# Optimization experiments

Hardware: AMD Instinct MI355X
Metric: run time of the kernel (lower is better)

The kernel has to match this reference:

```python
import jax, jax.numpy as jnp
import numpy as np
from jax import lax

B, H, W, C = 8, 72, 72, 16
HID_E, HID_P, T = 128, 16, 64
P_EPS = 1e-06
ALIVE_TH = 0.1

# Sobel kernels. The torch code runs conv on NCHW with spatial dims (D2, D1)
# (x.transpose(1,3)); in our NHWC layout spatial dims are (D1, D2), so the
# equivalent kernel is the transpose. With angle=0: w1 = dx, w2 = dy = dx.T.
_DX = np.outer([1.0, 2.0, 1.0], [-1.0, 0.0, 1.0]) / 8.0
_W1_EFF = _DX.T            # transpose of w1
_W2_EFF = _DX              # transpose of w2 (= dy.T)


def _depthwise(x, k2d):
    c = x.shape[-1]
    ker = jnp.tile(jnp.asarray(k2d, x.dtype)[:, :, None, None], (1, 1, 1, c))  # HWIO (3,3,1,C)
    return lax.conv_general_dilated(x, ker, (1, 1), 'SAME',
                                    feature_group_count=c,
                                    dimension_numbers=('NHWC', 'HWIO', 'NHWC'))


def _conv2d(x, w, b):
    y = lax.conv_general_dilated(x, w, (1, 1), 'SAME',
                                 dimension_numbers=('NHWC', 'HWIO', 'NHWC'))
    return y + b


def _maxpool3(a):  # a: (B,H,W)
    return lax.reduce_window(a, -jnp.inf, lax.max, (1, 3, 3), (1, 1, 1),
                             [(0, 0), (1, 1), (1, 1)])


def setup_inputs() -> dict:
    key = jax.random.key(0)
    ks = jax.random.split(key, 6)
    c3 = 3 * C
    x = jax.random.uniform(ks[0], (B, H, W, C), jnp.float32)
    conv1_w = jax.random.normal(ks[1], (3, 3, c3, HID_P), jnp.float32) * (1.0 / np.sqrt(9 * c3))
    conv1_b = jnp.zeros((HID_P,), jnp.float32)
    conv2_w = jax.random.normal(ks[2], (3, 3, HID_P, 1), jnp.float32) * (1.0 / np.sqrt(9 * HID_P))
    conv2_b = jnp.zeros((1,), jnp.float32)
    fc0_w = jax.random.normal(ks[3], (c3, HID_E), jnp.float32) * (1.0 / np.sqrt(c3))
    fc0_b = jnp.zeros((HID_E,), jnp.float32)
    fc1_w = jax.random.normal(ks[4], (HID_E, C), jnp.float32) * 0.01  # torch init is zeros; small random for a non-degenerate baseline
    return dict(x=x, conv1_w=conv1_w, conv1_b=conv1_b, conv2_w=conv2_w,
                conv2_b=conv2_b, fc0_w=fc0_w, fc0_b=fc0_b, fc1_w=fc1_w)


def reference(x, conv1_w, conv1_b, conv2_w, conv2_b, fc0_w, fc0_b, fc1_w):
    base_key = jax.random.key(42)

    def perceive(x):  # (B,H,W,C) -> (B,H,W,3C)
        return jnp.concatenate([x, _depthwise(x, _W1_EFF), _depthwise(x, _W2_EFF)], axis=-1)

    def lambda_net(perc):  # (B,H,W,3C) -> (B,H,W)
        h = jax.nn.relu(_conv2d(perc, conv1_w, conv1_b))
        return jax.nn.sigmoid(_conv2d(h, conv2_w, conv2_b))[..., 0]

    def alive(x):  # alpha channel index 3
        return _maxpool3(x[..., 3]) > ALIVE_TH

    def update(x, lambdas, key):
        pre = alive(x)
        perc = perceive(x)
        dx = jax.nn.relu(perc @ fc0_w + fc0_b) @ fc1_w  # pointwise MLP, fc1 has no bias
        upd = 1.0 - jax.random.bernoulli(key, lambdas).astype(x.dtype)  # (B,H,W)
        xn = x + dx * upd[..., None]
        life = (pre & alive(xn)).astype(x.dtype)[..., None]
        return xn * life, upd, perc

    # initial perceive/lambda/update (step 0)
    perc0 = perceive(x)
    lam0 = lambda_net(perc0)
    x0, upd0, perc = update(x, lam0, jax.random.fold_in(base_key, 0))
    un0 = jnp.ones((x.shape[0], H, W), x.dtype)

    def step(carry, n):
        xc, updc, percc, un = carry
        lam = lambda_net(percc)
        p_n = un * lam + P_EPS
        out = (xc, p_n, lam, updc)
        un = un * (1.0 - lam)
        xn, updn, percn = update(xc, lam, jax.random.fold_in(base_key, n))
        return (xn, updn, percn, un), out

    _, (x_steps, p_steps, lam_steps, upd_steps) = lax.scan(
        step, (x0, upd0, perc, un0), jnp.arange(1, T + 1))
    p_norm = p_steps / jnp.sum(p_steps, axis=0)
    return x_steps, p_norm, lam_steps, upd_steps
```

## Files before the change

kernel.cpp:

```cpp
#include <hip/hip_runtime.h>
#include <cstdint>
#include <cmath>

#define B_    8
#define H_    72
#define W_    72
#define C_    16
#define C3_   48
#define HP_   16
#define HE_   128
#define T_    64
#define NCELL 41472
#define NEDGE 2272

__host__ __device__ __forceinline__ void threefry2x32(uint32_t k0, uint32_t k1,
                                                      uint32_t& x0, uint32_t& x1) {
  uint32_t ks2 = k0 ^ k1 ^ 0x1BD11BDAu;
  x0 += k0; x1 += k1;
#define TF_R(r) { x0 += x1; x1 = (x1 << (r)) | (x1 >> (32 - (r))); x1 ^= x0; }
  TF_R(13) TF_R(15) TF_R(26) TF_R(6)
  x0 += k1; x1 += ks2 + 1u;
  TF_R(17) TF_R(29) TF_R(16) TF_R(24)
  x0 += ks2; x1 += k0 + 2u;
  TF_R(13) TF_R(15) TF_R(26) TF_R(6)
  x0 += k0; x1 += k1 + 3u;
  TF_R(17) TF_R(29) TF_R(16) TF_R(24)
  x0 += k1; x1 += ks2 + 4u;
  TF_R(13) TF_R(15) TF_R(26) TF_R(6)
  x0 += ks2; x1 += k0 + 5u;
#undef TF_R
}

__global__ void k_init(const float* __restrict__ xin, double* __restrict__ xA,
                       double* __restrict__ un) {
  int idx = blockIdx.x * 256 + threadIdx.x;
  if (idx < NCELL * C_) xA[idx] = (double)xin[idx];
  if (idx < NCELL) un[idx] = 1.0;
}

__global__ void k_prep(const float* __restrict__ w1, const float* __restrict__ b1,
                       const float* __restrict__ f0w, const float* __restrict__ f0b,
                       const float* __restrict__ f1w, const float* __restrict__ w2,
                       double* __restrict__ weffd, double* __restrict__ b1d,
                       double* __restrict__ fc0t, double* __restrict__ fc1d,
                       double* __restrict__ w2d, double* __restrict__ f0bd,
                       double* __restrict__ w1d) {
  int gid = blockIdx.x * 256 + threadIdx.x;
  const int stride = 26 * 256;
  for (int t = gid; t < 6400; t += stride) {
    int oc = t & 15;
    int c  = (t >> 4) & 15;
    int pos = t >> 8;
    int u = pos / 5, v = pos % 5;
    double acc = 0.0;
    for (int ei = 0; ei < 3; ei++) {
      int di = u - ei; if (di < 0 || di > 2) continue;
      for (int ej = 0; ej < 3; ej++) {
        int dj = v - ej; if (dj < 0 || dj > 2) continue;
        const float* wb = w1 + (size_t)((ei * 3 + ej) * C3_) * HP_ + oc;
        if (di == 1 && dj == 1) acc += (double)wb[c * HP_];
        double rf1 = (di == 0) ? -0.125 : (di == 2) ? 0.125 : 0.0;
        if (rf1 != 0.0) {
          double cf1 = (dj == 1) ? 2.0 : 1.0;
          acc += (double)wb[(C_ + c) * HP_] * (rf1 * cf1);
        }
        double cf2 = (dj == 0) ? -0.125 : (dj == 2) ? 0.125 : 0.0;
        if (cf2 != 0.0) {
          double rf2 = (di == 1) ? 2.0 : 1.0;
          acc += (double)wb[(2 * C_ + c) * HP_] * (cf2 * rf2);
        }
      }
    }
    weffd[t] = acc;
  }
  for (int t = gid; t < C3_ * HE_; t += stride) {
    int k = t >> 7, e = t & 127;
    fc0t[e * C3_ + k] = (double)f0w[t];
  }
  for (int t = gid; t < HE_ * C_; t += stride) fc1d[t] = (double)f1w[t];
  for (int t = gid; t < 144; t += stride) w2d[t] = (double)w2[t];
  for (int t = gid; t < HE_; t += stride) f0bd[t] = (double)f0b[t];
  for (int t = gid; t < HP_; t += stride) b1d[t] = (double)b1[t];
  for (int t = gid; t < 3 * 3 * C3_ * HP_; t += stride) w1d[t] = (double)w1[t];
}

__global__ void __launch_bounds__(256) k_conv1(const double* __restrict__ x,
    const double* __restrict__ weffd, const double* __restrict__ b1d,
    const double* __restrict__ w1d, double* __restrict__ hbuf) {
  int lane = threadIdx.x & 63;
  int wv = __builtin_amdgcn_readfirstlane(threadIdx.x >> 6);
  if (blockIdx.x < 324) {
    int gw = blockIdx.x * 4 + wv;
    int cellw = gw >> 1;
    int ocb = (gw & 1) << 3;
    int cell = (cellw << 6) + lane;
    int j = cell % W_; int t2 = cell / W_; int i = t2 % H_; int b = t2 / H_;
    if (i == 0 || i == H_ - 1 || j == 0 || j == W_ - 1) return;
    double acc[8];
#pragma unroll
    for (int o = 0; o < 8; o++) acc[o] = b1d[ocb + o];
#pragma unroll 1
    for (int u = 0; u < 5; u++) {
      int ii = i + u - 2; if (ii < 0 || ii >= H_) continue;
#pragma unroll 1
      for (int v = 0; v < 5; v++) {
        int jj = j + v - 2; if (jj < 0 || jj >= W_) continue;
        const double* xp = x + ((size_t)((b * H_ + ii) * W_ + jj) << 4);
        const double* wp = weffd + (u * 5 + v) * 256 + ocb;
        double xv[16];
#pragma unroll
        for (int ic = 0; ic < 16; ic++) xv[ic] = xp[ic];
#pragma unroll
        for (int ic = 0; ic < 16; ic++) {
#pragma unroll
          for (int o = 0; o < 8; o++)
            acc[o] = fma(xv[ic], wp[ic * 16 + o], acc[o]);
        }
      }
    }
    double* hp = hbuf + ((size_t)cell << 4) + ocb;
#pragma unroll
    for (int o = 0; o < 8; o++) hp[o] = acc[o] > 0.0 ? acc[o] : 0.0;
  } else {
    int gw = (blockIdx.x - 324) * 4 + wv;
    int oc = gw & 15;
    int grp = gw >> 4;
    int ecell = (grp << 6) + lane;
    if (ecell >= NEDGE) return;
    int b = ecell / 284, r = ecell % 284;
    int i, j;
    if (r < 72)       { i = 0;       j = r; }
    else if (r < 144) { i = H_ - 1;  j = r - 72; }
    else if (r < 214) { i = r - 143; j = 0; }
    else              { i = r - 213; j = W_ - 1; }
    int cell = (b * H_ + i) * W_ + j;
    double acc = b1d[oc];
    for (int ei = 0; ei < 3; ei++) {
      int pi = i + ei - 1; if (pi < 0 || pi >= H_) continue;
      for (int ej = 0; ej < 3; ej++) {
        int pj = j + ej - 1; if (pj < 0 || pj >= W_) continue;
        const double* wb = w1d + (size_t)((ei * 3 + ej) * C3_) * HP_ + oc;
        for (int c = 0; c < C_; c++) {
          double v[3][3];
#pragma unroll
          for (int a2 = 0; a2 < 3; a2++) {
#pragma unroll
            for (int b2i = 0; b2i < 3; b2i++) {
              int ii2 = pi + a2 - 1, jj2 = pj + b2i - 1;
              bool ok = (ii2 >= 0 && ii2 < H_ && jj2 >= 0 && jj2 < W_);
              v[a2][b2i] = ok ? x[(((size_t)((b * H_ + ii2) * W_ + jj2)) << 4) + c] : 0.0;
            }
          }
          double ctr = v[1][1];
          double dw1 = (-v[0][0] - 2.0 * v[0][1] - v[0][2] + v[2][0] + 2.0 * v[2][1] + v[2][2]) * 0.125;
          double dw2 = (-v[0][0] + v[0][2] - 2.0 * v[1][0] + 2.0 * v[1][2] - v[2][0] + v[2][2]) * 0.125;
          acc += ctr * wb[c * HP_] + dw1 * wb[(C_ + c) * HP_] + dw2 * wb[(2 * C_ + c) * HP_];
        }
      }
    }
    hbuf[((size_t)cell << 4) + oc] = acc > 0.0 ? acc : 0.0;
  }
}

__global__ void __launch_bounds__(128) k_upd(
    const double* __restrict__ x, const double* __restrict__ hbuf,
    const double* __restrict__ lamPrev, const double* __restrict__ fc0t,
    const double* __restrict__ fc1d, const double* __restrict__ w2d,
    const double* __restrict__ f0bd, const float* __restrict__ b2,
    double* __restrict__ lamNext, double* __restrict__ xn,
    float* __restrict__ out_upd, double* __restrict__ un,
    float* __restrict__ out_lam, double* __restrict__ p_buf,
    uint32_t k0, uint32_t k1, int n) {
  __shared__ double sdx[64][17];
  int lane = threadIdx.x & 63;
  int wv = __builtin_amdgcn_readfirstlane(threadIdx.x >> 6);
  int cell = (blockIdx.x << 6) + lane;
  int j = cell % W_; int t2 = cell / W_; int i = t2 % H_; int b = t2 / H_;

  double pv[C3_];
#pragma unroll
  for (int k = 0; k < C3_; k++) pv[k] = 0.0;
#pragma unroll
  for (int p = 0; p < 9; p++) {
    const int di = p / 3, dj = p % 3;
    const double k1c = (di == 0 ? -0.125 : di == 2 ? 0.125 : 0.0) * (dj == 1 ? 2.0 : 1.0);
    const double k2c = (dj == 0 ? -0.125 : dj == 2 ? 0.125 : 0.0) * (di == 1 ? 2.0 : 1.0);
    int ii = i + di - 1, jj = j + dj - 1;
    if (ii < 0 || ii >= H_ || jj < 0 || jj >= W_) continue;
    const double* xp = x + ((size_t)((b * H_ + ii) * W_ + jj) << 4);
#pragma unroll
    for (int c = 0; c < C_; c++) {
      double xv = xp[c];
      if (p == 4) pv[c] += xv;
      if (k1c != 0.0) pv[C_ + c] = fma(k1c, xv, pv[C_ + c]);
      if (k2c != 0.0) pv[2 * C_ + c] = fma(k2c, xv, pv[2 * C_ + c]);
    }
  }

  double dx[C_];
#pragma unroll
  for (int c = 0; c < C_; c++) dx[c] = 0.0;
  int ebase = wv << 6;
#pragma unroll 2
  for (int eg = 0; eg < 64; eg += 4) {
    const double* wrow = fc0t + (size_t)(ebase + eg) * C3_;
    double a0 = f0bd[ebase + eg + 0];
    double a1 = f0bd[ebase + eg + 1];
    double a2 = f0bd[ebase + eg + 2];
    double a3 = f0bd[ebase + eg + 3];
#pragma unroll
    for (int k = 0; k < C3_; k++) {
      a0 = fma(pv[k], wrow[k], a0);
      a1 = fma(pv[k], wrow[C3_ + k], a1);
      a2 = fma(pv[k], wrow[2 * C3_ + k], a2);
      a3 = fma(pv[k], wrow[3 * C3_ + k], a3);
    }
    a0 = a0 > 0.0 ? a0 : 0.0;
    a1 = a1 > 0.0 ? a1 : 0.0;
    a2 = a2 > 0.0 ? a2 : 0.0;
    a3 = a3 > 0.0 ? a3 : 0.0;
    const double* v0 = fc1d + ((size_t)(ebase + eg) << 4);
#pragma unroll
    for (int c = 0; c < C_; c++) {
      double s = fma(a0, v0[c], dx[c]);
      s = fma(a1, v0[16 + c], s);
      s = fma(a2, v0[32 + c], s);
      s = fma(a3, v0[48 + c], s);
      dx[c] = s;
    }
  }

  if (wv == 1) {
#pragma unroll
    for (int c = 0; c < C_; c++) sdx[lane][c] = dx[c];
  }
  __syncthreads();
  if (wv == 1) return;

#pragma unroll
  for (int c = 0; c < C_; c++) dx[c] += sdx[lane][c];

  double z = (double)b2[0];
  for (int di = 0; di < 3; di++) {
    int ii = i + di - 1; if (ii < 0 || ii >= H_) continue;
    for (int dj = 0; dj < 3; dj++) {
      int jj = j + dj - 1; if (jj < 0 || jj >= W_) continue;
      const double* hh = hbuf + ((size_t)((b * H_ + ii) * W_ + jj) << 4);
      const double* ww = w2d + (di * 3 + dj) * HP_;
#pragma unroll
      for (int ic = 0; ic < HP_; ic++) z = fma(hh[ic], ww[ic], z);
    }
  }
  double lamF = 1.0 / (1.0 + exp(-z));
  lamNext[cell] = lamF;
  double l = (n == 0) ? lamF : lamPrev[cell];

  if (n >= 1) {
    size_t o = (size_t)(n - 1) * NCELL + cell;
    out_lam[o] = (float)l;
    double u = un[cell];
    p_buf[o] = u * l + 1e-6;
    un[cell] = u * (1.0 - l);
  }

  uint32_t r0 = 0u, r1 = (uint32_t)cell;
  threefry2x32(k0, k1, r0, r1);
  double uf = (double)(r0 ^ r1) * 0x1p-32;
  double upd = (uf < l) ? 0.0 : 1.0;
  out_upd[(size_t)n * NCELL + cell] = (float)upd;
  const double* xc = x + ((size_t)cell << 4);
  double* xo = xn + ((size_t)cell << 4);
#pragma unroll
  for (int c = 0; c < C_; c++) xo[c] = xc[c] + dx[c] * upd;
}

__global__ void k_life(const double* __restrict__ xold, const double* __restrict__ xn,
                       double* __restrict__ xout, float* __restrict__ out_x, int n) {
  int idx = blockIdx.x * 256 + threadIdx.x;
  int c = idx & 15;
  int cell = idx >> 4;
  int j = cell % W_; int t = cell / W_; int i = t % H_; int b = t / H_;
  double mo = -1e300, mn2 = -1e300;
  for (int di = -1; di <= 1; di++) {
    int ii = i + di; if (ii < 0 || ii >= H_) continue;
    for (int dj = -1; dj <= 1; dj++) {
      int jj = j + dj; if (jj < 0 || jj >= W_) continue;
      size_t nb = (size_t)((b * H_ + ii) * W_ + jj) * C_;
      double a0 = xold[nb + 3]; if (a0 > mo) mo = a0;
      double a1 = xn[nb + 3];   if (a1 > mn2) mn2 = a1;
    }
  }
  bool life = (mo > 0.1) && (mn2 > 0.1);
  double v = life ? xn[((size_t)cell << 4) + c] : 0.0;
  xout[((size_t)cell << 4) + c] = v;
  out_x[(size_t)n * NCELL * C_ + ((size_t)cell << 4) + c] = (float)v;
}

__global__ void k_emit(const double* __restrict__ lam, const double* __restrict__ un,
                       float* __restrict__ out_lam, double* __restrict__ p_buf) {
  int cell = blockIdx.x * 256 + threadIdx.x;
  double l = lam[cell];
  size_t o = (size_t)(T_ - 1) * NCELL + cell;
  out_lam[o] = (float)l;
  p_buf[o] = un[cell] * l + 1e-6;
}

__global__ void k_pnorm(const double* __restrict__ p_buf, float* __restrict__ out_p) {
  int cell = blockIdx.x * 256 + threadIdx.x;
  double s = 0.0;
  for (int t = 0; t < T_; t++) s += p_buf[(size_t)t * NCELL + cell];
  for (int t = 0; t < T_; t++)
    out_p[(size_t)t * NCELL + cell] = (float)(p_buf[(size_t)t * NCELL + cell] / s);
}

extern "C" void kernel_launch(void* const* d_in, const int* in_sizes, int n_in,
                              void* d_out, int out_size, void* d_ws, size_t ws_size,
                              hipStream_t stream) {
  const float* xin = (const float*)d_in[0];
  const float* w1  = (const float*)d_in[1];
  const float* b1  = (const float*)d_in[2];
  const float* w2  = (const float*)d_in[3];
  const float* b2  = (const float*)d_in[4];
  const float* f0w = (const float*)d_in[5];
  const float* f0b = (const float*)d_in[6];
  const float* f1w = (const float*)d_in[7];

  float* out     = (float*)d_out;
  float* out_x   = out;
  float* out_p   = out_x + (size_t)T_ * NCELL * C_;
  float* out_lam = out_p + (size_t)T_ * NCELL;
  float* out_upd = out_lam + (size_t)T_ * NCELL;

  double* ws    = (double*)d_ws;
  double* xA    = ws;
  double* xB    = xA + (size_t)NCELL * C_;
  double* xn    = xB + (size_t)NCELL * C_;
  double* hbuf  = xn + (size_t)NCELL * C_;
  double* lamA  = hbuf + (size_t)NCELL * HP_;
  double* lamB  = lamA + NCELL;
  double* un    = lamB + NCELL;
  double* p_buf = un + NCELL;
  double* weffd = p_buf + (size_t)T_ * NCELL;
  double* fc0t  = weffd + 6400;
  double* fc1d  = fc0t + HE_ * C3_;
  double* w2d   = fc1d + HE_ * C_;
  double* f0bd  = w2d + 144;
  double* b1d   = f0bd + HE_;
  double* w1d   = b1d + HP_;

  k_init<<<2592, 256, 0, stream>>>(xin, xA, un);
  k_prep<<<26, 256, 0, stream>>>(w1, b1, f0w, f0b, f1w, w2,
                                 weffd, b1d, fc0t, fc1d, w2d, f0bd, w1d);

  double* cur = lamA;
  double* nxt = lamB;

  for (int n = 0; n <= T_ - 1; n++) {
    k_conv1<<<468, 256, 0, stream>>>(xA, weffd, b1d, w1d, hbuf);
    uint32_t kx0 = 0u, kx1 = (uint32_t)n;
    threefry2x32(0u, 42u, kx0, kx1);
    k_upd<<<648, 128, 0, stream>>>(xA, hbuf, cur, fc0t, fc1d, w2d, f0bd, b2,
                                   (n == 0 ? cur : nxt), xn, out_upd, un,
                                   out_lam, p_buf, kx0, kx1, n);
    k_life<<<2592, 256, 0, stream>>>(xA, xn, xB, out_x, n);
    { double* t = xA; xA = xB; xB = t; }
    if (n >= 1) { double* t = cur; cur = nxt; nxt = t; }
  }

  k_emit<<<162, 256, 0, stream>>>(cur, un, out_lam, p_buf);
  k_pnorm<<<162, 256, 0, stream>>>(p_buf, out_p);
}
```

Baseline: 14.78 ms.

## Split conv1 taps and fc0 hidden units across more waves with LDS reduction

The interior conv1 path now gives each 64-cell group a 512-thread block whose eight waves split the 25 effective 5x5 taps into four chunks for each of two output-channel halves. Partial sums are combined through shared memory. k_upd likewise spreads the 128 hidden units over eight waves instead of two, and wave 0 reduces seven partial dx vectors from LDS. The aim is more wavefronts and shorter serial FP64 chains per cell, paid for with extra LDS traffic, a barrier, and idle waves during the reductions.

New measurement: 27.13 ms. 1.84x slower.

```diff
diff --git a/kernel.cpp b/kernel.cpp
--- a/kernel.cpp
+++ b/kernel.cpp
@@ -12,6 +12,8 @@
 #define T_    64
 #define NCELL 41472
 #define NEDGE 2272
+#define NCG   648
+#define RBLK  72
 
 __host__ __device__ __forceinline__ void threefry2x32(uint32_t k0, uint32_t k1,
                                                       uint32_t& x0, uint32_t& x1) {
@@ -84,45 +86,65 @@
   for (int t = gid; t < 3 * 3 * C3_ * HP_; t += stride) w1d[t] = (double)w1[t];
 }
 
-__global__ void __launch_bounds__(256) k_conv1(const double* __restrict__ x,
+template <int P0, int P1>
+__device__ __forceinline__ void conv1_chunk(const double* __restrict__ x,
+    const double* __restrict__ weffd, int i, int j, int b, int ocb,
+    double (&acc)[8]) {
+#pragma unroll
+  for (int p = P0; p < P1; ++p) {
+    const int u = p / 5, v = p % 5;
+    int ii = i + u - 2, jj = j + v - 2;
+    if (ii < 0 || ii >= H_ || jj < 0 || jj >= W_) continue;
+    const double* xp = x + ((size_t)((b * H_ + ii) * W_ + jj) << 4);
+    const double* wp = weffd + p * 256 + ocb;
+    double xv[16];
+#pragma unroll
+    for (int ic = 0; ic < 16; ic++) xv[ic] = xp[ic];
+#pragma unroll
+    for (int ic = 0; ic < 16; ic++) {
+#pragma unroll
+      for (int o = 0; o < 8; o++)
+        acc[o] = fma(xv[ic], wp[ic * 16 + o], acc[o]);
+    }
+  }
+}
+
+__global__ void __launch_bounds__(512) k_conv1(const double* __restrict__ x,
     const double* __restrict__ weffd, const double* __restrict__ b1d,
     const double* __restrict__ w1d, double* __restrict__ hbuf) {
+  __shared__ double part[8][64][9];
   int lane = threadIdx.x & 63;
   int wv = __builtin_amdgcn_readfirstlane(threadIdx.x >> 6);
-  if (blockIdx.x < 324) {
-    int gw = blockIdx.x * 4 + wv;
-    int cellw = gw >> 1;
-    int ocb = (gw & 1) << 3;
-    int cell = (cellw << 6) + lane;
+  if (blockIdx.x < NCG) {
+    int ocb = (wv & 1) << 3;
+    int kq  = wv >> 1;
+    int cell = blockIdx.x * 64 + lane;
     int j = cell % W_; int t2 = cell / W_; int i = t2 % H_; int b = t2 / H_;
-    if (i == 0 || i == H_ - 1 || j == 0 || j == W_ - 1) return;
     double acc[8];
 #pragma unroll
-    for (int o = 0; o < 8; o++) acc[o] = b1d[ocb + o];
-#pragma unroll 1
-    for (int u = 0; u < 5; u++) {
-      int ii = i + u - 2; if (ii < 0 || ii >= H_) continue;
-#pragma unroll 1
-      for (int v = 0; v < 5; v++) {
-        int jj = j + v - 2; if (jj < 0 || jj >= W_) continue;
-        const double* xp = x + ((size_t)((b * H_ + ii) * W_ + jj) << 4);
-        const double* wp = weffd + (u * 5 + v) * 256 + ocb;
-        double xv[16];
-#pragma unroll
-        for (int ic = 0; ic < 16; ic++) xv[ic] = xp[ic];
-#pragma unroll
-        for (int ic = 0; ic < 16; ic++) {
-#pragma unroll
-          for (int o = 0; o < 8; o++)
-            acc[o] = fma(xv[ic], wp[ic * 16 + o], acc[o]);
-        }
+    for (int o = 0; o < 8; o++) acc[o] = 0.0;
+    if (kq == 0)      conv1_chunk<0, 7>(x, weffd, i, j, b, ocb, acc);
+    else if (kq == 1) conv1_chunk<7, 13>(x, weffd, i, j, b, ocb, acc);
+    else if (kq == 2) conv1_chunk<13, 19>(x, weffd, i, j, b, ocb, acc);
+    else              conv1_chunk<19, 25>(x, weffd, i, j, b, ocb, acc);
+#pragma unroll
+    for (int o = 0; o < 8; o++) part[wv][lane][o] = acc[o];
+    __syncthreads();
+    if (wv < 2) {
+      bool interior = (i > 0 && i < H_ - 1 && j > 0 && j < W_ - 1);
+      double s[8];
+#pragma unroll
+      for (int o = 0; o < 8; o++)
+        s[o] = b1d[ocb + o] + part[wv][lane][o] + part[wv + 2][lane][o]
+             + part[wv + 4][lane][o] + part[wv + 6][lane][o];
+      if (interior) {
+        double* hp = hbuf + ((size_t)cell << 4) + ocb;
+#pragma unroll
+        for (int o = 0; o < 8; o++) hp[o] = s[o] > 0.0 ? s[o] : 0.0;
       }
     }
-    double* hp = hbuf + ((size_t)cell << 4) + ocb;
-#pragma unroll
-    for (int o = 0; o < 8; o++) hp[o] = acc[o] > 0.0 ? acc[o] : 0.0;
   } else {
-    int gw = (blockIdx.x - 324) * 4 + wv;
+    int gw = (blockIdx.x - NCG) * 8 + wv;
     int oc = gw & 15;
     int grp = gw >> 4;
     int ecell = (grp << 6) + lane;
@@ -162,7 +184,7 @@
   }
 }
 
-__global__ void __launch_bounds__(128) k_upd(
+__global__ void __launch_bounds__(512) k_upd(
     const double* __restrict__ x, const double* __restrict__ hbuf,
     const double* __restrict__ lamPrev, const double* __restrict__ fc0t,
     const double* __restrict__ fc1d, const double* __restrict__ w2d,
@@ -171,7 +193,7 @@
     float* __restrict__ out_upd, double* __restrict__ un,
     float* __restrict__ out_lam, double* __restrict__ p_buf,
     uint32_t k0, uint32_t k1, int n) {
-  __shared__ double sdx[64][17];
+  __shared__ double sdx[7][64][17];
   int lane = threadIdx.x & 63;
   int wv = __builtin_amdgcn_readfirstlane(threadIdx.x >> 6);
   int cell = (blockIdx.x << 6) + lane;
@@ -200,9 +222,9 @@
   double dx[C_];
 #pragma unroll
   for (int c = 0; c < C_; c++) dx[c] = 0.0;
-  int ebase = wv << 6;
-#pragma unroll 2
-  for (int eg = 0; eg < 64; eg += 4) {
+  int ebase = wv << 4;
+#pragma unroll 1
+  for (int eg = 0; eg < 16; eg += 4) {
     const double* wrow = fc0t + (size_t)(ebase + eg) * C3_;
     double a0 = f0bd[ebase + eg + 0];
     double a1 = f0bd[ebase + eg + 1];
@@ -230,15 +252,18 @@
     }
   }
 
-  if (wv == 1) {
-#pragma unroll
-    for (int c = 0; c < C_; c++) sdx[lane][c] = dx[c];
+  if (wv != 0) {
+#pragma unroll
+    for (int c = 0; c < C_; c++) sdx[wv - 1][lane][c] = dx[c];
   }
   __syncthreads();
-  if (wv == 1) return;
-
-#pragma unroll
-  for (int c = 0; c < C_; c++) dx[c] += sdx[lane][c];
+  if (wv != 0) return;
+
+#pragma unroll 1
+  for (int w = 0; w < 7; w++) {
+#pragma unroll
+    for (int c = 0; c < C_; c++) dx[c] += sdx[w][lane][c];
+  }
 
   double z = (double)b2[0];
   for (int di = 0; di < 3; di++) {
@@ -356,10 +381,10 @@
   double* nxt = lamB;
 
   for (int n = 0; n <= T_ - 1; n++) {
-    k_conv1<<<468, 256, 0, stream>>>(xA, weffd, b1d, w1d, hbuf);
+    k_conv1<<<NCG + RBLK, 512, 0, stream>>>(xA, weffd, b1d, w1d, hbuf);
     uint32_t kx0 = 0u, kx1 = (uint32_t)n;
     threefry2x32(0u, 42u, kx0, kx1);
-    k_upd<<<648, 128, 0, stream>>>(xA, hbuf, cur, fc0t, fc1d, w2d, f0bd, b2,
+    k_upd<<<NCG, 512, 0, stream>>>(xA, hbuf, cur, fc0t, fc1d, w2d, f0bd, b2,
                                    (n == 0 ? cur : nxt), xn, out_upd, un,
                                    out_lam, p_buf, kx0, kx1, n);
     k_life<<<2592, 256, 0, stream>>>(xA, xn, xB, out_x, n);
```

## Stage weights in LDS as floats and repartition conv1/update work across threads

Applied to the files above, without the earlier changes.

The conv1 kernel now stages the 5x5 effective weights in shared memory and maps one thread per cell and output channel, with ring cells handled inline. The update kernel uses four waves per block. Each wave computes a quarter of the perception channels and a partial lambda conv, then they exchange results through shared memory. The MLP weights are held in LDS as floats and widened to double on use, which removes most of the double weight conversion in the prep kernel. This aims to cut global weight traffic and raise parallelism, at the cost of more LDS usage, extra barriers and per-block weight reloads.

Result: slower. 15.49 ms (+4.8%).

```diff
diff --git a/kernel.cpp b/kernel.cpp
--- a/kernel.cpp
+++ b/kernel.cpp
@@ -11,7 +11,8 @@
 #define HE_   128
 #define T_    64
 #define NCELL 41472
-#define NEDGE 2272
+
+typedef __attribute__((ext_vector_type(2))) double d2;
 
 __host__ __device__ __forceinline__ void threefry2x32(uint32_t k0, uint32_t k1,
                                                       uint32_t& x0, uint32_t& x1) {
@@ -38,13 +39,8 @@
   if (idx < NCELL) un[idx] = 1.0;
 }
 
-__global__ void k_prep(const float* __restrict__ w1, const float* __restrict__ b1,
-                       const float* __restrict__ f0w, const float* __restrict__ f0b,
-                       const float* __restrict__ f1w, const float* __restrict__ w2,
-                       double* __restrict__ weffd, double* __restrict__ b1d,
-                       double* __restrict__ fc0t, double* __restrict__ fc1d,
-                       double* __restrict__ w2d, double* __restrict__ f0bd,
-                       double* __restrict__ w1d) {
+__global__ void k_prep(const float* __restrict__ w1, const float* __restrict__ f0w,
+                       double* __restrict__ weffd, float* __restrict__ fc0tf) {
   int gid = blockIdx.x * 256 + threadIdx.x;
   const int stride = 26 * 256;
   for (int t = gid; t < 6400; t += stride) {
@@ -75,71 +71,47 @@
   }
   for (int t = gid; t < C3_ * HE_; t += stride) {
     int k = t >> 7, e = t & 127;
-    fc0t[e * C3_ + k] = (double)f0w[t];
-  }
-  for (int t = gid; t < HE_ * C_; t += stride) fc1d[t] = (double)f1w[t];
-  for (int t = gid; t < 144; t += stride) w2d[t] = (double)w2[t];
-  for (int t = gid; t < HE_; t += stride) f0bd[t] = (double)f0b[t];
-  for (int t = gid; t < HP_; t += stride) b1d[t] = (double)b1[t];
-  for (int t = gid; t < 3 * 3 * C3_ * HP_; t += stride) w1d[t] = (double)w1[t];
-}
-
-__global__ void __launch_bounds__(256) k_conv1(const double* __restrict__ x,
-    const double* __restrict__ weffd, const double* __restrict__ b1d,
-    const double* __restrict__ w1d, double* __restrict__ hbuf) {
-  int lane = threadIdx.x & 63;
-  int wv = __builtin_amdgcn_readfirstlane(threadIdx.x >> 6);
-  if (blockIdx.x < 324) {
-    int gw = blockIdx.x * 4 + wv;
-    int cellw = gw >> 1;
-    int ocb = (gw & 1) << 3;
-    int cell = (cellw << 6) + lane;
-    int j = cell % W_; int t2 = cell / W_; int i = t2 % H_; int b = t2 / H_;
-    if (i == 0 || i == H_ - 1 || j == 0 || j == W_ - 1) return;
-    double acc[8];
-#pragma unroll
-    for (int o = 0; o < 8; o++) acc[o] = b1d[ocb + o];
-#pragma unroll 1
-    for (int u = 0; u < 5; u++) {
-      int ii = i + u - 2; if (ii < 0 || ii >= H_) continue;
-#pragma unroll 1
-      for (int v = 0; v < 5; v++) {
-        int jj = j + v - 2; if (jj < 0 || jj >= W_) continue;
-        const double* xp = x + ((size_t)((b * H_ + ii) * W_ + jj) << 4);
-        const double* wp = weffd + (u * 5 + v) * 256 + ocb;
-        double xv[16];
-#pragma unroll
-        for (int ic = 0; ic < 16; ic++) xv[ic] = xp[ic];
-#pragma unroll
-        for (int ic = 0; ic < 16; ic++) {
-#pragma unroll
-          for (int o = 0; o < 8; o++)
-            acc[o] = fma(xv[ic], wp[ic * 16 + o], acc[o]);
-        }
+    fc0tf[e * C3_ + k] = f0w[t];
+  }
+}
+
+__global__ void __launch_bounds__(512) k_conv1(const double* __restrict__ x,
+    const double* __restrict__ weffd, const float* __restrict__ w1f,
+    const float* __restrict__ b1f, double* __restrict__ hbuf) {
+  __shared__ double sw[6400];
+  for (int t = threadIdx.x; t < 6400; t += 512) sw[t] = weffd[t];
+  __syncthreads();
+  int oc = threadIdx.x & 15;
+  int cs = threadIdx.x >> 4;
+  int cell = blockIdx.x * 32 + cs;
+  int j = cell % W_; int t2 = cell / W_; int i = t2 % H_; int b = t2 / H_;
+  bool ring = (i == 0 || i == H_ - 1 || j == 0 || j == W_ - 1);
+  double acc = (double)b1f[oc];
+  if (!ring) {
+#pragma unroll
+    for (int p = 0; p < 25; p++) {
+      const int u = p / 5, v = p % 5;
+      int ii = i + u - 2, jj = j + v - 2;
+      bool ok = ((unsigned)ii < (unsigned)H_) && ((unsigned)jj < (unsigned)W_);
+      int iic = ok ? ii : 0;
+      int jjc = ok ? jj : 0;
+      const double* xp = x + (((size_t)((b * H_ + iic) * W_ + jjc)) << 4);
+      const double* wp = sw + p * 256 + oc;
+#pragma unroll
+      for (int g = 0; g < 8; g++) {
+        d2 xv = *(const d2*)(xp + 2 * g);
+        double x0 = ok ? xv.x : 0.0;
+        double x1 = ok ? xv.y : 0.0;
+        acc = fma(x0, wp[(2 * g) * 16], acc);
+        acc = fma(x1, wp[(2 * g + 1) * 16], acc);
       }
     }
-    double* hp = hbuf + ((size_t)cell << 4) + ocb;
-#pragma unroll
-    for (int o = 0; o < 8; o++) hp[o] = acc[o] > 0.0 ? acc[o] : 0.0;
   } else {
-    int gw = (blockIdx.x - 324) * 4 + wv;
-    int oc = gw & 15;
-    int grp = gw >> 4;
-    int ecell = (grp << 6) + lane;
-    if (ecell >= NEDGE) return;
-    int b = ecell / 284, r = ecell % 284;
-    int i, j;
-    if (r < 72)       { i = 0;       j = r; }
-    else if (r < 144) { i = H_ - 1;  j = r - 72; }
-    else if (r < 214) { i = r - 143; j = 0; }
-    else              { i = r - 213; j = W_ - 1; }
-    int cell = (b * H_ + i) * W_ + j;
-    double acc = b1d[oc];
     for (int ei = 0; ei < 3; ei++) {
       int pi = i + ei - 1; if (pi < 0 || pi >= H_) continue;
       for (int ej = 0; ej < 3; ej++) {
         int pj = j + ej - 1; if (pj < 0 || pj >= W_) continue;
-        const double* wb = w1d + (size_t)((ei * 3 + ej) * C3_) * HP_ + oc;
+        const float* wb = w1f + (size_t)((ei * 3 + ej) * C3_) * HP_ + oc;
         for (int c = 0; c < C_; c++) {
           double v[3][3];
 #pragma unroll
@@ -154,103 +126,149 @@
           double ctr = v[1][1];
           double dw1 = (-v[0][0] - 2.0 * v[0][1] - v[0][2] + v[2][0] + 2.0 * v[2][1] + v[2][2]) * 0.125;
           double dw2 = (-v[0][0] + v[0][2] - 2.0 * v[1][0] + 2.0 * v[1][2] - v[2][0] + v[2][2]) * 0.125;
-          acc += ctr * wb[c * HP_] + dw1 * wb[(C_ + c) * HP_] + dw2 * wb[(2 * C_ + c) * HP_];
+          acc += ctr * (double)wb[c * HP_] + dw1 * (double)wb[(C_ + c) * HP_] + dw2 * (double)wb[(2 * C_ + c) * HP_];
         }
       }
     }
-    hbuf[((size_t)cell << 4) + oc] = acc > 0.0 ? acc : 0.0;
-  }
-}
-
-__global__ void __launch_bounds__(128) k_upd(
+  }
+  hbuf[((size_t)cell << 4) + oc] = acc > 0.0 ? acc : 0.0;
+}
+
+__global__ void __launch_bounds__(256) k_upd(
     const double* __restrict__ x, const double* __restrict__ hbuf,
-    const double* __restrict__ lamPrev, const double* __restrict__ fc0t,
-    const double* __restrict__ fc1d, const double* __restrict__ w2d,
-    const double* __restrict__ f0bd, const float* __restrict__ b2,
+    const double* __restrict__ lamPrev, const float* __restrict__ fc0tf,
+    const float* __restrict__ f1w, const float* __restrict__ w2f,
+    const float* __restrict__ f0b, const float* __restrict__ b2,
     double* __restrict__ lamNext, double* __restrict__ xn,
     float* __restrict__ out_upd, double* __restrict__ un,
     float* __restrict__ out_lam, double* __restrict__ p_buf,
     uint32_t k0, uint32_t k1, int n) {
-  __shared__ double sdx[64][17];
-  int lane = threadIdx.x & 63;
-  int wv = __builtin_amdgcn_readfirstlane(threadIdx.x >> 6);
+  __shared__ float s0f[HE_ * C3_];
+  __shared__ float s1f[HE_ * C_];
+  __shared__ float sw2[144];
+  __shared__ float sb0[HE_];
+  __shared__ double upool[3264];
+  int tid = threadIdx.x;
+  for (int t = tid; t < HE_ * C3_; t += 256) s0f[t] = fc0tf[t];
+  for (int t = tid; t < HE_ * C_; t += 256) s1f[t] = f1w[t];
+  if (tid < 144) sw2[tid] = w2f[tid];
+  if (tid < HE_) sb0[tid] = f0b[tid];
+
+  int lane = tid & 63;
+  int wv = __builtin_amdgcn_readfirstlane(tid >> 6);
+  int c0 = wv * 4;
   int cell = (blockIdx.x << 6) + lane;
   int j = cell % W_; int t2 = cell / W_; int i = t2 % H_; int b = t2 / H_;
 
-  double pv[C3_];
-#pragma unroll
-  for (int k = 0; k < C3_; k++) pv[k] = 0.0;
+  double pvx0 = 0.0, pvx1 = 0.0, pvx2 = 0.0, pvx3 = 0.0;
+  double pw10 = 0.0, pw11 = 0.0, pw12 = 0.0, pw13 = 0.0;
+  double pw20 = 0.0, pw21 = 0.0, pw22 = 0.0, pw23 = 0.0;
 #pragma unroll
   for (int p = 0; p < 9; p++) {
     const int di = p / 3, dj = p % 3;
     const double k1c = (di == 0 ? -0.125 : di == 2 ? 0.125 : 0.0) * (dj == 1 ? 2.0 : 1.0);
     const double k2c = (dj == 0 ? -0.125 : dj == 2 ? 0.125 : 0.0) * (di == 1 ? 2.0 : 1.0);
     int ii = i + di - 1, jj = j + dj - 1;
-    if (ii < 0 || ii >= H_ || jj < 0 || jj >= W_) continue;
-    const double* xp = x + ((size_t)((b * H_ + ii) * W_ + jj) << 4);
-#pragma unroll
-    for (int c = 0; c < C_; c++) {
-      double xv = xp[c];
-      if (p == 4) pv[c] += xv;
-      if (k1c != 0.0) pv[C_ + c] = fma(k1c, xv, pv[C_ + c]);
-      if (k2c != 0.0) pv[2 * C_ + c] = fma(k2c, xv, pv[2 * C_ + c]);
-    }
-  }
+    bool ok = ((unsigned)ii < (unsigned)H_) && ((unsigned)jj < (unsigned)W_);
+    int iic = ok ? ii : 0;
+    int jjc = ok ? jj : 0;
+    const double* xp = x + (((size_t)((b * H_ + iic) * W_ + jjc)) << 4) + c0;
+    d2 xa = *(const d2*)xp;
+    d2 xb = *(const d2*)(xp + 2);
+    double xv0 = ok ? xa.x : 0.0;
+    double xv1 = ok ? xa.y : 0.0;
+    double xv2 = ok ? xb.x : 0.0;
+    double xv3 = ok ? xb.y : 0.0;
+    if (p == 4) { pvx0 += xv0; pvx1 += xv1; pvx2 += xv2; pvx3 += xv3; }
+    if (k1c != 0.0) {
+      pw10 = fma(k1c, xv0, pw10); pw11 = fma(k1c, xv1, pw11);
+      pw12 = fma(k1c, xv2, pw12); pw13 = fma(k1c, xv3, pw13);
+    }
+    if (k2c != 0.0) {
+      pw20 = fma(k2c, xv0, pw20); pw21 = fma(k2c, xv1, pw21);
+      pw22 = fma(k2c, xv2, pw22); pw23 = fma(k2c, xv3, pw23);
+    }
+  }
+  {
+    double* pr = upool + lane * 51;
+    pr[c0 + 0] = pvx0; pr[c0 + 1] = pvx1; pr[c0 + 2] = pvx2; pr[c0 + 3] = pvx3;
+    pr[16 + c0 + 0] = pw10; pr[16 + c0 + 1] = pw11; pr[16 + c0 + 2] = pw12; pr[16 + c0 + 3] = pw13;
+    pr[32 + c0 + 0] = pw20; pr[32 + c0 + 1] = pw21; pr[32 + c0 + 2] = pw22; pr[32 + c0 + 3] = pw23;
+  }
+  __syncthreads();
+
+  double z = (wv == 0) ? (double)b2[0] : 0.0;
+  for (int di = 0; di < 3; di++) {
+    int ii = i + di - 1; if (ii < 0 || ii >= H_) continue;
+    for (int dj = 0; dj < 3; dj++) {
+      int jj = j + dj - 1; if (jj < 0 || jj >= W_) continue;
+      const double* hh = hbuf + (((size_t)((b * H_ + ii) * W_ + jj)) << 4) + c0;
+      const float* ww = sw2 + (di * 3 + dj) * HP_ + c0;
+      d2 h0 = *(const d2*)hh;
+      d2 h1 = *(const d2*)(hh + 2);
+      z = fma(h0.x, (double)ww[0], z);
+      z = fma(h0.y, (double)ww[1], z);
+      z = fma(h1.x, (double)ww[2], z);
+      z = fma(h1.y, (double)ww[3], z);
+    }
+  }
+
+  double pv[C3_];
+#pragma unroll
+  for (int k = 0; k < C3_; k++) pv[k] = upool[lane * 51 + k];
 
   double dx[C_];
 #pragma unroll
   for (int c = 0; c < C_; c++) dx[c] = 0.0;
-  int ebase = wv << 6;
-#pragma unroll 2
-  for (int eg = 0; eg < 64; eg += 4) {
-    const double* wrow = fc0t + (size_t)(ebase + eg) * C3_;
-    double a0 = f0bd[ebase + eg + 0];
-    double a1 = f0bd[ebase + eg + 1];
-    double a2 = f0bd[ebase + eg + 2];
-    double a3 = f0bd[ebase + eg + 3];
+  int ebase = wv << 5;
+#pragma unroll 1
+  for (int eg = 0; eg < 32; eg += 4) {
+    int e = ebase + eg;
+    const float* w0 = s0f + e * C3_;
+    double a0 = (double)sb0[e + 0];
+    double a1 = (double)sb0[e + 1];
+    double a2 = (double)sb0[e + 2];
+    double a3 = (double)sb0[e + 3];
 #pragma unroll
     for (int k = 0; k < C3_; k++) {
-      a0 = fma(pv[k], wrow[k], a0);
-      a1 = fma(pv[k], wrow[C3_ + k], a1);
-      a2 = fma(pv[k], wrow[2 * C3_ + k], a2);
-      a3 = fma(pv[k], wrow[3 * C3_ + k], a3);
+      a0 = fma(pv[k], (double)w0[k], a0);
+      a1 = fma(pv[k], (double)w0[C3_ + k], a1);
+      a2 = fma(pv[k], (double)w0[2 * C3_ + k], a2);
+      a3 = fma(pv[k], (double)w0[3 * C3_ + k], a3);
     }
     a0 = a0 > 0.0 ? a0 : 0.0;
     a1 = a1 > 0.0 ? a1 : 0.0;
     a2 = a2 > 0.0 ? a2 : 0.0;
     a3 = a3 > 0.0 ? a3 : 0.0;
-    const double* v0 = fc1d + ((size_t)(ebase + eg) << 4);
+    const float* v0 = s1f + (e << 4);
 #pragma unroll
     for (int c = 0; c < C_; c++) {
-      double s = fma(a0, v0[c], dx[c]);
-      s = fma(a1, v0[16 + c], s);
-      s = fma(a2, v0[32 + c], s);
-      s = fma(a3, v0[48 + c], s);
+      double s = fma(a0, (double)v0[c], dx[c]);
+      s = fma(a1, (double)v0[16 + c], s);
+      s = fma(a2, (double)v0[32 + c], s);
+      s = fma(a3, (double)v0[48 + c], s);
       dx[c] = s;
     }
   }
 
-  if (wv == 1) {
-#pragma unroll
-    for (int c = 0; c < C_; c++) sdx[lane][c] = dx[c];
-  }
   __syncthreads();
-  if (wv == 1) return;
-
-#pragma unroll
-  for (int c = 0; c < C_; c++) dx[c] += sdx[lane][c];
-
-  double z = (double)b2[0];
-  for (int di = 0; di < 3; di++) {
-    int ii = i + di - 1; if (ii < 0 || ii >= H_) continue;
-    for (int dj = 0; dj < 3; dj++) {
-      int jj = j + dj - 1; if (jj < 0 || jj >= W_) continue;
-      const double* hh = hbuf + ((size_t)((b * H_ + ii) * W_ + jj) << 4);
-      const double* ww = w2d + (di * 3 + dj) * HP_;
-#pragma unroll
-      for (int ic = 0; ic < HP_; ic++) z = fma(hh[ic], ww[ic], z);
-    }
-  }
+  if (wv != 0) {
+    double* pr = upool + (wv - 1) * 1088 + lane * 17;
+#pragma unroll
+    for (int c = 0; c < C_; c++) pr[c] = dx[c];
+    pr[16] = z;
+  }
+  __syncthreads();
+  if (wv != 0) return;
+
+#pragma unroll
+  for (int w = 0; w < 3; w++) {
+    const double* pr = upool + w * 1088 + lane * 17;
+#pragma unroll
+    for (int c = 0; c < C_; c++) dx[c] += pr[c];
+    z += pr[16];
+  }
+
   double lamF = 1.0 / (1.0 + exp(-z));
   lamNext[cell] = lamF;
   double l = (n == 0) ? lamF : lamPrev[cell];
@@ -341,25 +359,19 @@
   double* un    = lamB + NCELL;
   double* p_buf = un + NCELL;
   double* weffd = p_buf + (size_t)T_ * NCELL;
-  double* fc0t  = weffd + 6400;
-  double* fc1d  = fc0t + HE_ * C3_;
-  double* w2d   = fc1d + HE_ * C_;
-  double* f0bd  = w2d + 144;
-  double* b1d   = f0bd + HE_;
-  double* w1d   = b1d + HP_;
+  float*  fc0tf = (float*)(weffd + 6400);
 
   k_init<<<2592, 256, 0, stream>>>(xin, xA, un);
-  k_prep<<<26, 256, 0, stream>>>(w1, b1, f0w, f0b, f1w, w2,
-                                 weffd, b1d, fc0t, fc1d, w2d, f0bd, w1d);
+  k_prep<<<26, 256, 0, stream>>>(w1, f0w, weffd, fc0tf);
 
   double* cur = lamA;
   double* nxt = lamB;
 
   for (int n = 0; n <= T_ - 1; n++) {
-    k_conv1<<<468, 256, 0, stream>>>(xA, weffd, b1d, w1d, hbuf);
+    k_conv1<<<1296, 512, 0, stream>>>(xA, weffd, w1, b1, hbuf);
     uint32_t kx0 = 0u, kx1 = (uint32_t)n;
     threefry2x32(0u, 42u, kx0, kx1);
-    k_upd<<<648, 128, 0, stream>>>(xA, hbuf, cur, fc0t, fc1d, w2d, f0bd, b2,
+    k_upd<<<648, 256, 0, stream>>>(xA, hbuf, cur, fc0tf, f1w, w2, f0b, b2,
                                    (n == 0 ? cur : nxt), xn, out_upd, un,
                                    out_lam, p_buf, kx0, kx1, n);
     k_life<<<2592, 256, 0, stream>>>(xA, xn, xB, out_x, n);
```
